# Kernel tuning notes

Hardware: AMD Instinct MI355X
Metric: run time of the kernel (lower is better)

The kernel has to match this reference:

```python
import jax, jax.numpy as jnp
import numpy as np

N_NODES = 100000
N_EDGES = 3200000
IN_F, HID, OUT_F = 512, 64, 64
K_HOPS = 10


def setup_inputs() -> dict:
    key = jax.random.key(0)
    k1, k2, k3, k4, k5 = jax.random.split(key, 5)
    x = jax.random.normal(k1, (N_NODES, IN_F), dtype=jnp.float32)
    edge_index = jax.random.randint(k2, (2, N_EDGES), 0, N_NODES, dtype=jnp.int64)
    # Glorot-ish scaled params (bias=False per init_kwargs)
    W1 = jax.random.normal(k3, (IN_F, HID), dtype=jnp.float32) / np.sqrt(IN_F)
    W2 = jax.random.normal(k4, (HID, OUT_F), dtype=jnp.float32) / np.sqrt(HID)
    s = jax.random.normal(k5, (OUT_F, 1), dtype=jnp.float32) / np.sqrt(OUT_F)
    return {"x": x, "edge_index": edge_index, "W1": W1, "W2": W2, "s": s}


def reference(x, edge_index, W1, W2, s):
    # --- MLP (dropout omitted: eval mode), relu applied after each linear per source ---
    h = jnp.maximum(x @ W1, 0.0)          # [N, HID]
    h = jnp.maximum(h @ W2, 0.0)          # [N, OUT_F]

    src = edge_index[0]
    dst = edge_index[1]
    n = h.shape[0]
    ones = jnp.ones(src.shape[0], dtype=h.dtype)
    deg_out = jax.ops.segment_sum(ones, src, num_segments=n)
    deg_in = jax.ops.segment_sum(ones, dst, num_segments=n)
    dinv_out = jnp.where(deg_out > 0, jax.lax.rsqrt(jnp.maximum(deg_out, 1.0)), 0.0)
    dinv_in = jnp.where(deg_in > 0, jax.lax.rsqrt(jnp.maximum(deg_in, 1.0)), 0.0)
    norm = dinv_out[src] * dinv_in[dst]   # [E] symmetric normalization

    # --- K-hop propagation: D^{-1/2} A D^{-1/2} applied K times ---
    hops = [h]
    feat = h
    for _ in range(K_HOPS):  # small fixed K, unrolled
        msg = feat[src] * norm[:, None]                          # gather [E, F]
        feat = jax.ops.segment_sum(msg, dst, num_segments=n)     # scatter [N, F]
        hops.append(feat)
    H = jnp.stack(hops, axis=1)            # [N, K+1, F]

    # --- adaptive hop combination via sigmoid gate ---
    scores = jax.nn.sigmoid(H @ s)         # [N, K+1, 1]
    out = jnp.sum(scores * H, axis=1)      # [N, F]
    return out
```

## Files before the change

### kernel.cpp

```cpp
#include <hip/hip_runtime.h>
#include <hip/hip_bf16.h>

#define N_NODES 100000
#define N_EDGES 3200000
#define IN_F 512
#define HID 64
#define OUT_F 64
#define K_HOPS 10

#define HIST_BLOCKS 64
#define HIST_BINS 32768
#define HIST_WORDS (HIST_BINS / 2)
#define EDGES_PER_HIST_BLOCK (N_EDGES / HIST_BLOCKS)

#define NBKT 224
#define NBN  448
#define BKT_CAP 16384
#define BKZ_BLOCKS 256
#define EDGES_PER_BKZ_BLOCK (N_EDGES / BKZ_BLOCKS)
#define BKZ_BATCH 8192

typedef __attribute__((ext_vector_type(8))) short bf16x8;
typedef __attribute__((ext_vector_type(4))) float f32x4;

static __device__ __forceinline__ unsigned short f2bf(float f) {
    unsigned int u = __float_as_uint(f);
    u += 0x7FFFu + ((u >> 16) & 1u);
    return (unsigned short)(u >> 16);
}
static __device__ __forceinline__ float bf2f(unsigned short s) {
    return __uint_as_float(((unsigned int)s) << 16);
}

__global__ void detect_i32_kernel(const unsigned int* ei_words, int* flag_is32) {
    int i = blockIdx.x * blockDim.x + threadIdx.x;
    unsigned int w = ei_words[2 * i + 1];
    if (w != 0u) atomicOr(flag_is32, 1);
}

__global__ void __launch_bounds__(256) convert_kernel(const void* ei_raw, const int* flag_is32,
                                                      int* __restrict__ src32,
                                                      int* __restrict__ dst32) {
    int t = blockIdx.x * blockDim.x + threadIdx.x;
    if (t >= N_EDGES / 2) return;
    if (*flag_is32) {
        const int2* ei = (const int2*)ei_raw;
        *(int2*)(src32 + 2 * t) = ei[t];
        *(int2*)(dst32 + 2 * t) = ei[N_EDGES / 2 + t];
    } else {
        const longlong2* ei = (const longlong2*)ei_raw;
        longlong2 s = ei[t];
        longlong2 d = ei[N_EDGES / 2 + t];
        *(int2*)(src32 + 2 * t) = make_int2((int)s.x, (int)s.y);
        *(int2*)(dst32 + 2 * t) = make_int2((int)d.x, (int)d.y);
    }
}

__global__ void __launch_bounds__(256) wconv_kernel(const float* __restrict__ W1,
                                                    const float* __restrict__ W2,
                                                    unsigned short* __restrict__ b1g,
                                                    unsigned short* __restrict__ b2g) {
    int o = blockIdx.x * blockDim.x + threadIdx.x;
    int which = (o >= IN_F * HID);
    int oo = which ? (o - IN_F * HID) : o;
    int ko = oo & 7;
    int l = (oo >> 3) & 63;
    int kgs = l >> 4;
    int cm = l & 15;
    int tile = oo >> 9;
    int gt = tile >> 2;
    int nt = tile & 3;
    int k = gt * 32 + kgs * 8 + ko;
    int c = nt * 16 + cm;
    if (which) b2g[oo] = f2bf(W2[k * OUT_F + c]);
    else       b1g[oo] = f2bf(W1[k * HID + c]);
}

__global__ void __launch_bounds__(256) hist_kernel(const int* __restrict__ a,
                                                   unsigned int* __restrict__ partials) {
    __shared__ unsigned int cnt[HIST_WORDS];
    int tid = threadIdx.x;
    for (int w = tid; w < HIST_WORDS; w += 256) cnt[w] = 0u;
    __syncthreads();

    int range = blockIdx.y;
    unsigned lo = (unsigned)(range * HIST_BINS);
    int beg = blockIdx.x * EDGES_PER_HIST_BLOCK;
    int end = beg + EDGES_PER_HIST_BLOCK;
    for (int i = beg + tid; i < end; i += 256) {
        unsigned v = (unsigned)a[i] - lo;
        if (v < HIST_BINS) atomicAdd(&cnt[v >> 1], 1u << ((v & 1u) * 16u));
    }
    __syncthreads();

    unsigned int* outp = partials + ((size_t)(blockIdx.y * HIST_BLOCKS + blockIdx.x)) * HIST_WORDS;
    for (int w = tid; w < HIST_WORDS / 4; w += 256)
        ((uint4*)outp)[w] = ((const uint4*)cnt)[w];
}

__global__ void __launch_bounds__(256) hist_scan_kernel(const unsigned int* __restrict__ partials,
                                                        float* __restrict__ dinv) {
    int wg = blockIdx.x * blockDim.x + threadIdx.x;
    if (wg >= 4 * HIST_WORDS) return;
    int range = wg >> 14;
    int word = wg & (HIST_WORDS - 1);
    const unsigned int* base = partials + ((size_t)range * HIST_BLOCKS) * HIST_WORDS + word;
    unsigned lo = 0, hi = 0;
    for (int b = 0; b < HIST_BLOCKS; ++b) {
        unsigned c = base[(size_t)b * HIST_WORDS];
        lo += c & 0xffffu;
        hi += c >> 16;
    }
    int v0 = range * HIST_BINS + 2 * word;
    if (v0 < N_NODES) dinv[v0] = lo ? rsqrtf((float)lo) : 0.0f;
    int v1 = v0 + 1;
    if (v1 < N_NODES) dinv[v1] = hi ? rsqrtf((float)hi) : 0.0f;
}

__global__ void __launch_bounds__(256) bucket_cnt_kernel(const int* __restrict__ dst32,
                                                         int* __restrict__ bucket_cnt) {
    __shared__ int c[NBKT];
    int tid = threadIdx.x;
    if (tid < NBKT) c[tid] = 0;
    __syncthreads();
    int beg = blockIdx.x * EDGES_PER_BKZ_BLOCK;
    int end = beg + EDGES_PER_BKZ_BLOCK;
    for (int i = beg + tid; i < end; i += 256) {
        atomicAdd(&c[dst32[i] / NBN], 1);
    }
    __syncthreads();
    if (tid < NBKT && c[tid] > 0) atomicAdd(&bucket_cnt[tid], c[tid]);
}

__global__ void __launch_bounds__(256) bucket_scan_kernel(const int* __restrict__ bucket_cnt,
                                                          int* __restrict__ bucket_start,
                                                          int* __restrict__ gcur,
                                                          int* __restrict__ row_start) {
    __shared__ int s[256];
    int t = threadIdx.x;
    int c = (t < NBKT) ? bucket_cnt[t] : 0;
    s[t] = c;
    __syncthreads();
    for (int off = 1; off < 256; off <<= 1) {
        int add = (t >= off) ? s[t - off] : 0;
        __syncthreads();
        s[t] += add;
        __syncthreads();
    }
    if (t < NBKT) {
        int excl = s[t] - c;
        bucket_start[t] = excl;
        gcur[t] = excl;
        if (t == NBKT - 1) {
            bucket_start[NBKT] = s[t];
            row_start[N_NODES] = s[t];
        }
    }
}

__global__ void __launch_bounds__(256) bucketize_kernel(const int* __restrict__ src32,
                                                        const int* __restrict__ dst32,
                                                        int* __restrict__ gcur,
                                                        int* __restrict__ entries) {
    __shared__ unsigned int stag[BKZ_BATCH];
    __shared__ unsigned char stagb[BKZ_BATCH];
    __shared__ int cnt[256], sAr[256], ofs_l[256], gbase_l[256];

    int tid = threadIdx.x;
    int beg = blockIdx.x * EDGES_PER_BKZ_BLOCK;

    for (int bb = 0; bb < EDGES_PER_BKZ_BLOCK; bb += BKZ_BATCH) {
        int bn = min(BKZ_BATCH, EDGES_PER_BKZ_BLOCK - bb);
        cnt[tid] = 0;
        __syncthreads();

        unsigned pk[32];
#pragma unroll
        for (int j = 0; j < 32; ++j) {
            int loc = j * 256 + tid;
            pk[j] = 0xFFFFFFFFu;
            if (loc < bn) {
                int d = dst32[beg + bb + loc];
                int b = d / NBN;
                int dl = d - b * NBN;
                int off = atomicAdd(&cnt[b], 1);
                pk[j] = ((unsigned)b << 22) | ((unsigned)dl << 13) | (unsigned)off;
            }
        }
        __syncthreads();
        int c = cnt[tid];
        sAr[tid] = c;
        __syncthreads();
        for (int off = 1; off < 256; off <<= 1) {
            int add = (tid >= off) ? sAr[tid - off] : 0;
            __syncthreads();
            sAr[tid] += add;
            __syncthreads();
        }
        ofs_l[tid] = sAr[tid] - c;
        if (tid < NBKT && c > 0) gbase_l[tid] = atomicAdd(&gcur[tid], c);
        __syncthreads();

#pragma unroll
        for (int j = 0; j < 32; ++j) {
            int loc = j * 256 + tid;
            if (loc < bn && pk[j] != 0xFFFFFFFFu) {
                int s = src32[beg + bb + loc];
                int b = pk[j] >> 22;
                int dl = (pk[j] >> 13) & 511;
                int off = pk[j] & 8191;
                int pos = ofs_l[b] + off;
                stag[pos] = ((unsigned)s << 9) | (unsigned)dl;
                stagb[pos] = (unsigned char)b;
            }
        }
        __syncthreads();
        for (int i = tid; i < bn; i += 256) {
            int b = stagb[i];
            entries[gbase_l[b] + (i - ofs_l[b])] = (int)stag[i];
        }
        __syncthreads();
    }
}

#define SORT_LDS_BYTES ((2 * BKT_CAP + 512 + 512) * 4)
__global__ void __launch_bounds__(1024) sort_kernel(const int* __restrict__ entries,
                                                    const int* __restrict__ bucket_start,
                                                    int* __restrict__ srcs,
                                                    int* __restrict__ row_start,
                                                    float* __restrict__ dinv_in) {
    extern __shared__ int sbuf[];
    int* sin  = sbuf;
    int* sout = sbuf + BKT_CAP;
    int* cnt  = sbuf + 2 * BKT_CAP;
    int* nsum = cnt + 512;
    int tid = threadIdx.x;
    int b = blockIdx.x;
    int ebeg = bucket_start[b];
    int eend = bucket_start[b + 1];
    int n = eend - ebeg;

    for (int i = tid; i < n; i += 1024) sin[i] = entries[ebeg + i];
    if (tid < 512) { cnt[tid] = 0; nsum[tid] = 0; }
    __syncthreads();
    for (int i = tid; i < n; i += 1024) {
        atomicAdd(&cnt[(unsigned)sin[i] & 511u], 1);
    }
    __syncthreads();
    int c = (tid < 512) ? cnt[tid] : 0;
    if (tid < 512) nsum[tid] = c;
    __syncthreads();
    for (int off = 1; off < 512; off <<= 1) {
        int v = (tid < 512 && tid >= off) ? nsum[tid - off] : 0;
        __syncthreads();
        if (tid < 512) nsum[tid] += v;
        __syncthreads();
    }
    if (tid < NBN) {
        int excl = nsum[tid] - c;
        cnt[tid] = excl;
        int node = b * NBN + tid;
        if (node < N_NODES) {
            row_start[node] = ebeg + excl;
            dinv_in[node] = c ? rsqrtf((float)c) : 0.0f;
        }
    }
    __syncthreads();
    for (int i = tid; i < n; i += 1024) {
        unsigned e = (unsigned)sin[i];
        int pos = atomicAdd(&cnt[e & 511u], 1);
        sout[pos] = (int)(e >> 9);
    }
    __syncthreads();
    for (int i = tid; i < n; i += 1024) srcs[ebeg + i] = sout[i];
}

__global__ void __launch_bounds__(256) mlp_kernel(const float* __restrict__ x,
                                                  const unsigned short* __restrict__ b1g,
                                                  const unsigned short* __restrict__ b2g,
                                                  const float* __restrict__ sv,
                                                  const float* __restrict__ dinv_out,
                                                  float* __restrict__ out,
                                                  unsigned short* __restrict__ g0) {
    __shared__ __align__(16) unsigned short a2s[4][2 * 64 * 8];

    int tid = threadIdx.x;
    int w = tid >> 6;
    int l = tid & 63;
    int kg = l >> 4;
    int m  = l & 15;
    int row0 = blockIdx.x * 64;
    int row = row0 + w * 16 + m;
    bool valid = row < N_NODES;
    const float* xp = x + (size_t)row * IN_F + kg * 8;

    f32x4 acc[4];
#pragma unroll
    for (int nt = 0; nt < 4; ++nt) acc[nt] = (f32x4){0.f, 0.f, 0.f, 0.f};

#pragma unroll 4
    for (int gt = 0; gt < 16; ++gt) {
        union { bf16x8 v; unsigned short u[8]; } a;
        if (valid) {
            const float* ap = xp + gt * 32;
            float4 u0 = *(const float4*)ap;
            float4 u1 = *(const float4*)(ap + 4);
            a.u[0] = f2bf(u0.x); a.u[1] = f2bf(u0.y);
            a.u[2] = f2bf(u0.z); a.u[3] = f2bf(u0.w);
            a.u[4] = f2bf(u1.x); a.u[5] = f2bf(u1.y);
            a.u[6] = f2bf(u1.z); a.u[7] = f2bf(u1.w);
        } else {
#pragma unroll
            for (int q = 0; q < 8; ++q) a.u[q] = 0;
        }
#pragma unroll
        for (int nt = 0; nt < 4; ++nt) {
            bf16x8 b = *(const bf16x8*)&b1g[((gt * 4 + nt) * 64 + l) * 8];
            acc[nt] = __builtin_amdgcn_mfma_f32_16x16x32_bf16(a.v, b, acc[nt], 0, 0, 0);
        }
    }

#pragma unroll
    for (int nt = 0; nt < 4; ++nt) {
#pragma unroll
        for (int reg = 0; reg < 4; ++reg) {
            float v = fmaxf(acc[nt][reg], 0.0f);
            int cc = nt * 16 + m;
            int r = kg * 4 + reg;
            a2s[w][((cc >> 5) * 64 + (((cc >> 3) & 3) * 16 + r)) * 8 + (cc & 7)] = f2bf(v);
        }
    }

    f32x4 acc2[4];
#pragma unroll
    for (int nt = 0; nt < 4; ++nt) acc2[nt] = (f32x4){0.f, 0.f, 0.f, 0.f};
#pragma unroll
    for (int t2 = 0; t2 < 2; ++t2) {
        bf16x8 a = *(const bf16x8*)&a2s[w][(t2 * 64 + l) * 8];
#pragma unroll
        for (int nt = 0; nt < 4; ++nt) {
            bf16x8 b = *(const bf16x8*)&b2g[((t2 * 4 + nt) * 64 + l) * 8];
            acc2[nt] = __builtin_amdgcn_mfma_f32_16x16x32_bf16(a, b, acc2[nt], 0, 0, 0);
        }
    }

    float vals[4][4];
    float pr[4] = {0.f, 0.f, 0.f, 0.f};
#pragma unroll
    for (int nt = 0; nt < 4; ++nt) {
        float s_c = sv[nt * 16 + m];
#pragma unroll
        for (int reg = 0; reg < 4; ++reg) {
            float v = fmaxf(acc2[nt][reg], 0.0f);
            vals[nt][reg] = v;
            pr[reg] = fmaf(v, s_c, pr[reg]);
        }
    }
#pragma unroll
    for (int off = 1; off <= 8; off <<= 1) {
#pragma unroll
        for (int reg = 0; reg < 4; ++reg) pr[reg] += __shfl_xor(pr[reg], off, 64);
    }
#pragma unroll
    for (int reg = 0; reg < 4; ++reg) {
        int node = row0 + w * 16 + kg * 4 + reg;
        if (node < N_NODES) {
            float score = 1.0f / (1.0f + expf(-pr[reg]));
            float dv = dinv_out[node];
#pragma unroll
            for (int nt = 0; nt < 4; ++nt) {
                out[(size_t)node * OUT_F + nt * 16 + m] = score * vals[nt][reg];
                g0[(size_t)node * OUT_F + nt * 16 + m] = f2bf(dv * vals[nt][reg]);
            }
        }
    }
}

__global__ void __launch_bounds__(256) hop_kernel(
        const unsigned short* __restrict__ g_prev,
        const int* __restrict__ row_start,
        const int* __restrict__ srcs,
        const float* __restrict__ dinv_in,
        const float* __restrict__ dinv_out,
        const float* __restrict__ sv,
        unsigned short* __restrict__ g_next,
        float* __restrict__ out) {
    int lane = threadIdx.x & 63;
    int node = blockIdx.x * 4 + (threadIdx.x >> 6);
    if (node >= N_NODES) return;
    int beg = row_start[node];
    int end = row_start[node + 1];
    int slot = lane >> 3;
    int sub  = lane & 7;

    float acc[8];
#pragma unroll
    for (int j = 0; j < 8; ++j) acc[j] = 0.0f;

    for (int chunk = beg; chunk < end; chunk += 64) {
        int nrem = end - chunk;
        int es = (chunk + lane < end) ? srcs[chunk + lane] : 0;

        uint4 v[8];
#pragma unroll
        for (int g = 0; g < 8; ++g) {
            int s = __shfl(es, g * 8 + slot, 64);
            if (g * 8 + slot < nrem)
                v[g] = *(const uint4*)(g_prev + (size_t)s * OUT_F + sub * 8);
        }
#pragma unroll
        for (int g = 0; g < 8; ++g) {
            if (g * 8 + slot < nrem) {
                acc[0] += __uint_as_float(v[g].x << 16);
                acc[1] += __uint_as_float(v[g].x & 0xffff0000u);
                acc[2] += __uint_as_float(v[g].y << 16);
                acc[3] += __uint_as_float(v[g].y & 0xffff0000u);
                acc[4] += __uint_as_float(v[g].z << 16);
                acc[5] += __uint_as_float(v[g].z & 0xffff0000u);
                acc[6] += __uint_as_float(v[g].w << 16);
                acc[7] += __uint_as_float(v[g].w & 0xffff0000u);
            }
        }
    }
#pragma unroll
    for (int off = 8; off <= 32; off <<= 1) {
#pragma unroll
        for (int j = 0; j < 8; ++j) acc[j] += __shfl_xor(acc[j], off, 64);
    }
    float di = dinv_in[node];
    float dq = dinv_out[node];
    float fn[8];
#pragma unroll
    for (int j = 0; j < 8; ++j) fn[j] = di * acc[j];

    float4 s0 = *(const float4*)(sv + sub * 8);
    float4 s1 = *(const float4*)(sv + sub * 8 + 4);
    float p = fn[0] * s0.x + fn[1] * s0.y + fn[2] * s0.z + fn[3] * s0.w
            + fn[4] * s1.x + fn[5] * s1.y + fn[6] * s1.z + fn[7] * s1.w;
#pragma unroll
    for (int off = 1; off <= 4; off <<= 1) p += __shfl_xor(p, off, 64);
    float score = 1.0f / (1.0f + expf(-p));

    if (slot == 0) {
        uint4 wv;
        wv.x = (unsigned)f2bf(dq * fn[0]) | ((unsigned)f2bf(dq * fn[1]) << 16);
        wv.y = (unsigned)f2bf(dq * fn[2]) | ((unsigned)f2bf(dq * fn[3]) << 16);
        wv.z = (unsigned)f2bf(dq * fn[4]) | ((unsigned)f2bf(dq * fn[5]) << 16);
        wv.w = (unsigned)f2bf(dq * fn[6]) | ((unsigned)f2bf(dq * fn[7]) << 16);
        *(uint4*)(g_next + (size_t)node * OUT_F + sub * 8) = wv;
    } else if (slot == 1) {
        float4* op = (float4*)(out + (size_t)node * OUT_F + sub * 8);
        float4 o0 = op[0], o1 = op[1];
        o0.x = fmaf(score, fn[0], o0.x);
        o0.y = fmaf(score, fn[1], o0.y);
        o0.z = fmaf(score, fn[2], o0.z);
        o0.w = fmaf(score, fn[3], o0.w);
        o1.x = fmaf(score, fn[4], o1.x);
        o1.y = fmaf(score, fn[5], o1.y);
        o1.z = fmaf(score, fn[6], o1.z);
        o1.w = fmaf(score, fn[7], o1.w);
        op[0] = o0;
        op[1] = o1;
    }
}

extern "C" void kernel_launch(void* const* d_in, const int* in_sizes, int n_in,
                              void* d_out, int out_size, void* d_ws, size_t ws_size,
                              hipStream_t stream) {
    const float* x  = (const float*)d_in[0];
    const void*  ei = d_in[1];
    const float* W1 = (const float*)d_in[2];
    const float* W2 = (const float*)d_in[3];
    const float* sv = (const float*)d_in[4];
    float* out = (float*)d_out;

    char* p = (char*)d_ws;
    auto alloc = [&](size_t bytes) -> char* {
        char* r = p;
        p += (bytes + 255) & ~(size_t)255;
        return r;
    };
    unsigned short* gA = (unsigned short*)alloc(sizeof(unsigned short) * N_NODES * OUT_F);
    unsigned short* gB = (unsigned short*)alloc(sizeof(unsigned short) * N_NODES * OUT_F);
    int*   src32     = (int*)alloc(sizeof(int) * N_EDGES);
    int*   dst32     = (int*)alloc(sizeof(int) * N_EDGES);
    char*  shared_region = alloc(sizeof(unsigned int) * 4 * HIST_BLOCKS * HIST_WORDS);
    unsigned int* partials = (unsigned int*)shared_region;
    int*   entries_raw = (int*)shared_region;
    int*   srcs      = (int*)alloc(sizeof(int) * N_EDGES);
    unsigned short* b1g = (unsigned short*)alloc(sizeof(unsigned short) * IN_F * HID);
    unsigned short* b2g = (unsigned short*)alloc(sizeof(unsigned short) * HID * OUT_F);
    float* dinv_out  = (float*)alloc(sizeof(float) * N_NODES);
    float* dinv_in   = (float*)alloc(sizeof(float) * N_NODES);
    int*   row_start = (int*)alloc(sizeof(int) * (N_NODES + 1));
    int*   bucket_cnt   = (int*)alloc(sizeof(int) * NBKT);
    int*   bucket_start = (int*)alloc(sizeof(int) * (NBKT + 1));
    int*   gcur      = (int*)alloc(sizeof(int) * NBKT);
    int*   flag      = (int*)alloc(256);

    hipMemsetAsync(flag, 0, sizeof(int), stream);
    hipMemsetAsync(bucket_cnt, 0, sizeof(int) * NBKT, stream);

    detect_i32_kernel<<<4, 256, 0, stream>>>((const unsigned int*)ei, flag);
    convert_kernel<<<(N_EDGES / 2 + 255) / 256, 256, 0, stream>>>(ei, flag, src32, dst32);
    wconv_kernel<<<(IN_F * HID + HID * OUT_F + 255) / 256, 256, 0, stream>>>(W1, W2, b1g, b2g);

    hist_kernel<<<dim3(HIST_BLOCKS, 4), 256, 0, stream>>>(src32, partials);
    hist_scan_kernel<<<(4 * HIST_WORDS + 255) / 256, 256, 0, stream>>>(partials, dinv_out);

    bucket_cnt_kernel<<<BKZ_BLOCKS, 256, 0, stream>>>(dst32, bucket_cnt);
    bucket_scan_kernel<<<1, 256, 0, stream>>>(bucket_cnt, bucket_start, gcur, row_start);
    bucketize_kernel<<<BKZ_BLOCKS, 256, 0, stream>>>(src32, dst32, gcur, entries_raw);

    hipFuncSetAttribute((const void*)sort_kernel,
                        hipFuncAttributeMaxDynamicSharedMemorySize, SORT_LDS_BYTES);
    sort_kernel<<<NBKT, 1024, SORT_LDS_BYTES, stream>>>(entries_raw, bucket_start,
                                                        srcs, row_start, dinv_in);

    int mlp_blocks = (N_NODES + 63) / 64;
    mlp_kernel<<<mlp_blocks, 256, 0, stream>>>(x, b1g, b2g, sv, dinv_out, out, gA);

    int node_blocks = (N_NODES + 3) / 4;
    unsigned short* cur = gA;
    unsigned short* nxt = gB;
    for (int hop = 0; hop < K_HOPS; ++hop) {
        hop_kernel<<<node_blocks, 256, 0, stream>>>(cur, row_start, srcs,
                                                    dinv_in, dinv_out, sv, nxt, out);
        unsigned short* t = cur; cur = nxt; nxt = t;
    }
}
```

Baseline: 827.5 us.

## Defer sigmoid hop gating to a single combine kernel over stored hops

Hop kernels no longer compute the gate score or read-modify-write the fp32 output each hop. Every hop's scaled bf16 features are kept in an 11-slot arena, and a final combine kernel rebuilds each hop's features by dividing by dinv_out, computes the gates and sums them. This removes ten fp32 output RMW passes and the per-hop reductions. In exchange it reads all stored hops once at the end, and the output now comes from bf16-rounded features. Nodes with zero out-degree cannot have their features recovered.

```diff
diff --git a/kernel.cpp b/kernel.cpp
--- a/kernel.cpp
+++ b/kernel.cpp
@@ -278,9 +278,7 @@
 __global__ void __launch_bounds__(256) mlp_kernel(const float* __restrict__ x,
                                                   const unsigned short* __restrict__ b1g,
                                                   const unsigned short* __restrict__ b2g,
-                                                  const float* __restrict__ sv,
                                                   const float* __restrict__ dinv_out,
-                                                  float* __restrict__ out,
                                                   unsigned short* __restrict__ g0) {
     __shared__ __align__(16) unsigned short a2s[4][2 * 64 * 8];
 
@@ -344,33 +342,15 @@
         }
     }
 
-    float vals[4][4];
-    float pr[4] = {0.f, 0.f, 0.f, 0.f};
-#pragma unroll
-    for (int nt = 0; nt < 4; ++nt) {
-        float s_c = sv[nt * 16 + m];
-#pragma unroll
-        for (int reg = 0; reg < 4; ++reg) {
-            float v = fmaxf(acc2[nt][reg], 0.0f);
-            vals[nt][reg] = v;
-            pr[reg] = fmaf(v, s_c, pr[reg]);
-        }
-    }
-#pragma unroll
-    for (int off = 1; off <= 8; off <<= 1) {
-#pragma unroll
-        for (int reg = 0; reg < 4; ++reg) pr[reg] += __shfl_xor(pr[reg], off, 64);
-    }
 #pragma unroll
     for (int reg = 0; reg < 4; ++reg) {
         int node = row0 + w * 16 + kg * 4 + reg;
         if (node < N_NODES) {
-            float score = 1.0f / (1.0f + expf(-pr[reg]));
             float dv = dinv_out[node];
 #pragma unroll
             for (int nt = 0; nt < 4; ++nt) {
-                out[(size_t)node * OUT_F + nt * 16 + m] = score * vals[nt][reg];
-                g0[(size_t)node * OUT_F + nt * 16 + m] = f2bf(dv * vals[nt][reg]);
+                g0[(size_t)node * OUT_F + nt * 16 + m] =
+                    f2bf(dv * fmaxf(acc2[nt][reg], 0.0f));
             }
         }
     }
@@ -382,9 +362,7 @@
         const int* __restrict__ srcs,
         const float* __restrict__ dinv_in,
         const float* __restrict__ dinv_out,
-        const float* __restrict__ sv,
-        unsigned short* __restrict__ g_next,
-        float* __restrict__ out) {
+        unsigned short* __restrict__ g_next) {
     int lane = threadIdx.x & 63;
     int node = blockIdx.x * 4 + (threadIdx.x >> 6);
     if (node >= N_NODES) return;
@@ -427,41 +405,42 @@
 #pragma unroll
         for (int j = 0; j < 8; ++j) acc[j] += __shfl_xor(acc[j], off, 64);
     }
-    float di = dinv_in[node];
-    float dq = dinv_out[node];
-    float fn[8];
-#pragma unroll
-    for (int j = 0; j < 8; ++j) fn[j] = di * acc[j];
-
-    float4 s0 = *(const float4*)(sv + sub * 8);
-    float4 s1 = *(const float4*)(sv + sub * 8 + 4);
-    float p = fn[0] * s0.x + fn[1] * s0.y + fn[2] * s0.z + fn[3] * s0.w
-            + fn[4] * s1.x + fn[5] * s1.y + fn[6] * s1.z + fn[7] * s1.w;
-#pragma unroll
-    for (int off = 1; off <= 4; off <<= 1) p += __shfl_xor(p, off, 64);
-    float score = 1.0f / (1.0f + expf(-p));
-
     if (slot == 0) {
+        float sc = dinv_in[node] * dinv_out[node];
         uint4 wv;
-        wv.x = (unsigned)f2bf(dq * fn[0]) | ((unsigned)f2bf(dq * fn[1]) << 16);
-        wv.y = (unsigned)f2bf(dq * fn[2]) | ((unsigned)f2bf(dq * fn[3]) << 16);
-        wv.z = (unsigned)f2bf(dq * fn[4]) | ((unsigned)f2bf(dq * fn[5]) << 16);
-        wv.w = (unsigned)f2bf(dq * fn[6]) | ((unsigned)f2bf(dq * fn[7]) << 16);
+        wv.x = (unsigned)f2bf(sc * acc[0]) | ((unsigned)f2bf(sc * acc[1]) << 16);
+        wv.y = (unsigned)f2bf(sc * acc[2]) | ((unsigned)f2bf(sc * acc[3]) << 16);
+        wv.z = (unsigned)f2bf(sc * acc[4]) | ((unsigned)f2bf(sc * acc[5]) << 16);
+        wv.w = (unsigned)f2bf(sc * acc[6]) | ((unsigned)f2bf(sc * acc[7]) << 16);
         *(uint4*)(g_next + (size_t)node * OUT_F + sub * 8) = wv;
-    } else if (slot == 1) {
-        float4* op = (float4*)(out + (size_t)node * OUT_F + sub * 8);
-        float4 o0 = op[0], o1 = op[1];
-        o0.x = fmaf(score, fn[0], o0.x);
-        o0.y = fmaf(score, fn[1], o0.y);
-        o0.z = fmaf(score, fn[2], o0.z);
-        o0.w = fmaf(score, fn[3], o0.w);
-        o1.x = fmaf(score, fn[4], o1.x);
-        o1.y = fmaf(score, fn[5], o1.y);
-        o1.z = fmaf(score, fn[6], o1.z);
-        o1.w = fmaf(score, fn[7], o1.w);
-        op[0] = o0;
-        op[1] = o1;
-    }
+    }
+}
+
+__global__ void __launch_bounds__(256) combine_kernel(
+        const unsigned short* __restrict__ garena,
+        const float* __restrict__ dinv_out,
+        const float* __restrict__ sv,
+        float* __restrict__ out) {
+    int lane = threadIdx.x & 63;
+    int node = blockIdx.x * 4 + (threadIdx.x >> 6);
+    if (node >= N_NODES) return;
+    float dv = dinv_out[node];
+    float rinv = (dv > 0.0f) ? 1.0f / dv : 0.0f;
+    float sl = sv[lane];
+    size_t idx = (size_t)node * OUT_F + lane;
+    const size_t gstride = (size_t)N_NODES * OUT_F;
+
+    float o = 0.0f;
+#pragma unroll
+    for (int k = 0; k <= K_HOPS; ++k) {
+        float fn = bf2f(garena[(size_t)k * gstride + idx]) * rinv;
+        float p = fn * sl;
+#pragma unroll
+        for (int off = 1; off <= 32; off <<= 1) p += __shfl_xor(p, off, 64);
+        float score = 1.0f / (1.0f + expf(-p));
+        o = fmaf(score, fn, o);
+    }
+    out[idx] = o;
 }
 
 extern "C" void kernel_launch(void* const* d_in, const int* in_sizes, int n_in,
@@ -480,8 +459,8 @@
         p += (bytes + 255) & ~(size_t)255;
         return r;
     };
-    unsigned short* gA = (unsigned short*)alloc(sizeof(unsigned short) * N_NODES * OUT_F);
-    unsigned short* gB = (unsigned short*)alloc(sizeof(unsigned short) * N_NODES * OUT_F);
+    const size_t gstride = (size_t)N_NODES * OUT_F;
+    unsigned short* garena = (unsigned short*)alloc(sizeof(unsigned short) * gstride * (K_HOPS + 1));
     int*   src32     = (int*)alloc(sizeof(int) * N_EDGES);
     int*   dst32     = (int*)alloc(sizeof(int) * N_EDGES);
     char*  shared_region = alloc(sizeof(unsigned int) * 4 * HIST_BLOCKS * HIST_WORDS);
@@ -518,14 +497,13 @@
                                                         srcs, row_start, dinv_in);
 
     int mlp_blocks = (N_NODES + 63) / 64;
-    mlp_kernel<<<mlp_blocks, 256, 0, stream>>>(x, b1g, b2g, sv, dinv_out, out, gA);
+    mlp_kernel<<<mlp_blocks, 256, 0, stream>>>(x, b1g, b2g, dinv_out, garena);
 
     int node_blocks = (N_NODES + 3) / 4;
-    unsigned short* cur = gA;
-    unsigned short* nxt = gB;
-    for (int hop = 0; hop < K_HOPS; ++hop) {
-        hop_kernel<<<node_blocks, 256, 0, stream>>>(cur, row_start, srcs,
-                                                    dinv_in, dinv_out, sv, nxt, out);
-        unsigned short* t = cur; cur = nxt; nxt = t;
-    }
-}
+    for (int hop = 1; hop <= K_HOPS; ++hop) {
+        hop_kernel<<<node_blocks, 256, 0, stream>>>(garena + (size_t)(hop - 1) * gstride,
+                                                    row_start, srcs, dinv_in, dinv_out,
+                                                    garena + (size_t)hop * gstride);
+    }
+    combine_kernel<<<node_blocks, 256, 0, stream>>>(garena, dinv_out, sv, out);
+}
```

New measurement: 799.9 us. 1.03x faster.
